# Kernel tuning notes

Hardware: AMD Instinct MI355X
Metric: run time of the kernel (lower is better)

The kernel has to match this reference:

```python
import jax, jax.numpy as jnp
import numpy as np

N, E, D, L = 100000, 640000, 128, 5
BN_EPS = 1e-5


def setup_inputs() -> dict:
    key = jax.random.key(0)
    ks = jax.random.split(key, 10)
    x = jax.random.normal(ks[0], (N, D), jnp.float32)
    edge_index = jax.random.randint(ks[1], (2, E), 0, N, dtype=jnp.int32)
    W1 = jax.random.normal(ks[2], (L, D, 2 * D), jnp.float32) / np.float32(np.sqrt(D))
    b1 = jnp.zeros((L, 2 * D), jnp.float32)
    bn1_g = jnp.ones((L, 2 * D), jnp.float32)
    bn1_b = jnp.zeros((L, 2 * D), jnp.float32)
    bn1_m = 0.1 * jax.random.normal(ks[3], (L, 2 * D), jnp.float32)
    bn1_v = jax.random.uniform(ks[4], (L, 2 * D), jnp.float32) + 0.5
    W2 = jax.random.normal(ks[5], (L, 2 * D, D), jnp.float32) / np.float32(np.sqrt(2 * D))
    b2 = jnp.zeros((L, D), jnp.float32)
    bno_g = jnp.ones((L, D), jnp.float32)
    bno_b = jnp.zeros((L, D), jnp.float32)
    bno_m = 0.1 * jax.random.normal(ks[6], (L, D), jnp.float32)
    bno_v = jax.random.uniform(ks[7], (L, D), jnp.float32) + 0.5
    return {"x": x, "edge_index": edge_index, "W1": W1, "b1": b1,
            "bn1_g": bn1_g, "bn1_b": bn1_b, "bn1_m": bn1_m, "bn1_v": bn1_v,
            "W2": W2, "b2": b2,
            "bno_g": bno_g, "bno_b": bno_b, "bno_m": bno_m, "bno_v": bno_v}


def _bn(z, g, b, m, v):
    # BatchNorm1d in eval mode: running stats
    return (z - m) * jax.lax.rsqrt(v + BN_EPS) * g + b


def reference(x, edge_index, W1, b1, bn1_g, bn1_b, bn1_m, bn1_v,
              W2, b2, bno_g, bno_b, bno_m, bno_v):
    src, dst = edge_index[0], edge_index[1]
    h = x
    for l in range(L):
        # GINConv with eps=0: (1+eps)*h_i + sum_{j->i} h_j
        agg = h + jax.ops.segment_sum(h[src], dst, num_segments=N)  # [N, d]
        z = jax.nn.relu(_bn(agg @ W1[l] + b1[l], bn1_g[l], bn1_b[l], bn1_m[l], bn1_v[l]))
        h = _bn(z @ W2[l] + b2[l], bno_g[l], bno_b[l], bno_m[l], bno_v[l])
        if l != L - 1:
            h = jax.nn.relu(h)
        # dropout is identity in eval mode
    return h
```

## Files before the change

kernel.cpp:

```cpp
#include <hip/hip_runtime.h>

#define ND 100000
#define DD 128
#define HH 256
#define EE 640000
#define LL 5

typedef __attribute__((ext_vector_type(8))) short short8;
typedef __attribute__((ext_vector_type(4))) short short4v;
typedef __attribute__((ext_vector_type(4))) float f32x4;

static __device__ __forceinline__ short f2bf(float f) {
    unsigned u = __builtin_bit_cast(unsigned, f);
    unsigned r = (u + 0x7fffu + ((u >> 16) & 1u)) >> 16;
    return (short)r;
}
static __device__ __forceinline__ float bf2f(short s) {
    unsigned u = ((unsigned)(unsigned short)s) << 16;
    return __builtin_bit_cast(float, u);
}

__global__ __launch_bounds__(256) void setup(
    const float* __restrict__ W1, const float* __restrict__ b1,
    const float* __restrict__ g1, const float* __restrict__ bb1,
    const float* __restrict__ m1, const float* __restrict__ v1,
    const float* __restrict__ W2, const float* __restrict__ b2,
    const float* __restrict__ g2, const float* __restrict__ bb2,
    const float* __restrict__ m2, const float* __restrict__ v2,
    const float* __restrict__ x, const int* __restrict__ dst,
    short* __restrict__ W1p, float* __restrict__ b1e,
    short* __restrict__ W2p, float* __restrict__ b2e,
    short* __restrict__ hb, int* __restrict__ cnt)
{
    int bx = blockIdx.x;
    int tid = threadIdx.x;
    if (bx < 640) {
        int id = bx * 256 + tid;
        if (id < LL * HH * DD) {
            int l = id >> 15;
            int rem = id & 32767;
            {
                int n = rem >> 7, k = rem & 127;
                float s = g1[l * HH + n] * rsqrtf(v1[l * HH + n] + 1e-5f);
                W1p[id] = f2bf(W1[l * 32768 + k * HH + n] * s);
            }
            {
                int n2 = rem >> 8, k2 = rem & 255;
                float s = g2[l * DD + n2] * rsqrtf(v2[l * DD + n2] + 1e-5f);
                W2p[id] = f2bf(W2[l * 32768 + k2 * DD + n2] * s);
            }
        }
        if (id < LL * HH) {
            float s = g1[id] * rsqrtf(v1[id] + 1e-5f);
            b1e[id] = (b1[id] - m1[id]) * s + bb1[id];
        }
        if (id < LL * DD) {
            float s = g2[id] * rsqrtf(v2[id] + 1e-5f);
            b2e[id] = (b2[id] - m2[id]) * s + bb2[id];
        }
    } else if (bx < 13140) {
        int i = (bx - 640) * 256 + tid;
        float4 v = reinterpret_cast<const float4*>(x)[i];
        short4v s;
        s.x = f2bf(v.x); s.y = f2bf(v.y); s.z = f2bf(v.z); s.w = f2bf(v.w);
        reinterpret_cast<short4v*>(hb)[i] = s;
    } else {
        int e = (bx - 13140) * 256 + tid;
        if (e < EE) atomicAdd(&cnt[dst[e]], 1);
    }
}

__global__ __launch_bounds__(256) void scan_block(int* __restrict__ cnt, int* __restrict__ bsum)
{
    __shared__ int buf[256];
    int tid = threadIdx.x;
    int idx = blockIdx.x * 256 + tid;
    int v = (idx < ND) ? cnt[idx] : 0;
    buf[tid] = v;
    __syncthreads();
    int sum = v;
    for (int off = 1; off < 256; off <<= 1) {
        int t = (tid >= off) ? buf[tid - off] : 0;
        __syncthreads();
        sum += t;
        buf[tid] = sum;
        __syncthreads();
    }
    if (idx < ND) cnt[idx] = sum;
    if (tid == 255) bsum[blockIdx.x] = sum;
}

__global__ __launch_bounds__(256) void apply_offs2(const int* __restrict__ cnt,
                                                   const int* __restrict__ bsum,
                                                   int* __restrict__ rowst)
{
    __shared__ int sred[256];
    int tid = threadIdx.x;
    int partial = 0;
    for (int i = tid; i < blockIdx.x; i += 256) partial += bsum[i];
    sred[tid] = partial;
    __syncthreads();
    for (int off = 128; off > 0; off >>= 1) {
        if (tid < off) sred[tid] += sred[tid + off];
        __syncthreads();
    }
    int boff = sred[0];
    int idx = blockIdx.x * 256 + tid;
    if (idx < ND) rowst[idx + 1] = cnt[idx] + boff;
    if (idx == 0) rowst[0] = 0;
}

__global__ __launch_bounds__(256) void fill_csr(const int* __restrict__ src,
                                                const int* __restrict__ dst,
                                                const int* __restrict__ rowstart,
                                                int* __restrict__ cursor,
                                                int* __restrict__ csr)
{
    int e = blockIdx.x * 256 + threadIdx.x;
    if (e < EE) {
        int d = dst[e];
        int p = atomicAdd(&cursor[d], 1);
        csr[rowstart[d] + p] = src[e];
    }
}

__global__ __launch_bounds__(1024, 8) void layer_fused(
    const short* __restrict__ hb_in,
    const int* __restrict__ rowst,
    const int* __restrict__ csr,
    const short* __restrict__ W1l,
    const float* __restrict__ b1l,
    const short* __restrict__ W2l,
    const float* __restrict__ b2l,
    short* __restrict__ hb_out, float* __restrict__ f_out, int last)
{
    __shared__ __attribute__((aligned(16))) short sU[64 * 264];

    const int tid = threadIdx.x;
    const int r0 = blockIdx.x * 64;
    const int wave = tid >> 6;
    const int lane = tid & 63;
    const int quad = lane >> 4;
    const int l16 = lane & 15;

    const int zrow = wave * 16 + l16;
    short8 aw1[4];
    for (int ks = 0; ks < 4; ++ks)
        aw1[ks] = *reinterpret_cast<const short8*>(&W1l[zrow * DD + ks * 32 + quad * 8]);
    float4 bias1 = *reinterpret_cast<const float4*>(&b1l[wave * 16 + quad * 4]);

    {
        int row = tid >> 4;
        int ch = (tid & 15) * 8;
        int grow = r0 + row;
        float acc[8];
        if (grow < ND) {
            short8 h0 = *reinterpret_cast<const short8*>(&hb_in[(size_t)grow * DD + ch]);
            for (int j = 0; j < 8; ++j) acc[j] = bf2f(h0[j]);
            int s = rowst[grow], e = rowst[grow + 1];
            int i = s;
            for (; i + 3 < e; i += 4) {
                int s0 = csr[i], s1 = csr[i + 1], s2 = csr[i + 2], s3 = csr[i + 3];
                short8 a0 = *reinterpret_cast<const short8*>(&hb_in[(size_t)s0 * DD + ch]);
                short8 a1 = *reinterpret_cast<const short8*>(&hb_in[(size_t)s1 * DD + ch]);
                short8 a2 = *reinterpret_cast<const short8*>(&hb_in[(size_t)s2 * DD + ch]);
                short8 a3 = *reinterpret_cast<const short8*>(&hb_in[(size_t)s3 * DD + ch]);
                for (int j = 0; j < 8; ++j)
                    acc[j] += (bf2f(a0[j]) + bf2f(a1[j])) + (bf2f(a2[j]) + bf2f(a3[j]));
            }
            for (; i < e; ++i) {
                short8 a = *reinterpret_cast<const short8*>(&hb_in[(size_t)csr[i] * DD + ch]);
                for (int j = 0; j < 8; ++j) acc[j] += bf2f(a[j]);
            }
        } else {
            for (int j = 0; j < 8; ++j) acc[j] = 0.f;
        }
        short8 o;
        for (int j = 0; j < 8; ++j) o[j] = f2bf(acc[j]);
        *reinterpret_cast<short8*>(&sU[row * 136 + ch]) = o;
    }
    __syncthreads();

    const f32x4 zero4 = {0.f, 0.f, 0.f, 0.f};
    f32x4 acc1[4];
    for (int nt = 0; nt < 4; ++nt) acc1[nt] = zero4;

    for (int ks = 0; ks < 4; ++ks) {
        int kofs = ks * 32 + quad * 8;
        for (int nt = 0; nt < 4; ++nt) {
            short8 bn = *reinterpret_cast<const short8*>(&sU[(nt * 16 + l16) * 136 + kofs]);
            acc1[nt] = __builtin_amdgcn_mfma_f32_16x16x32_bf16(aw1[ks], bn, acc1[nt], 0, 0, 0);
        }
    }
    __syncthreads();

    {
        int zc = wave * 16 + quad * 4;
        for (int nt = 0; nt < 4; ++nt) {
            int node = nt * 16 + l16;
            short4v o;
            o.x = f2bf(fmaxf(acc1[nt][0] + bias1.x, 0.f));
            o.y = f2bf(fmaxf(acc1[nt][1] + bias1.y, 0.f));
            o.z = f2bf(fmaxf(acc1[nt][2] + bias1.z, 0.f));
            o.w = f2bf(fmaxf(acc1[nt][3] + bias1.w, 0.f));
            *reinterpret_cast<short4v*>(&sU[node * 264 + zc]) = o;
        }
    }

    const int ct16 = wave >> 1;
    const int nh = wave & 1;
    const int orow = ct16 * 16 + l16;
    short8 w_cur = *reinterpret_cast<const short8*>(&W2l[orow * HH + quad * 8]);
    float4 bias2 = *reinterpret_cast<const float4*>(&b2l[ct16 * 16 + quad * 4]);
    __syncthreads();

    f32x4 acc2[2];
    for (int nt = 0; nt < 2; ++nt) acc2[nt] = zero4;

    for (int ks = 0; ks < 8; ++ks) {
        short8 w_next;
        if (ks < 7)
            w_next = *reinterpret_cast<const short8*>(&W2l[orow * HH + (ks + 1) * 32 + quad * 8]);
        int kofs = ks * 32 + quad * 8;
        for (int nt = 0; nt < 2; ++nt) {
            int node = nh * 32 + nt * 16 + l16;
            short8 bn = *reinterpret_cast<const short8*>(&sU[node * 264 + kofs]);
            acc2[nt] = __builtin_amdgcn_mfma_f32_16x16x32_bf16(w_cur, bn, acc2[nt], 0, 0, 0);
        }
        w_cur = w_next;
    }

    {
        int oc = ct16 * 16 + quad * 4;
        for (int nt = 0; nt < 2; ++nt) {
            int node = r0 + nh * 32 + nt * 16 + l16;
            if (node < ND) {
                float v0 = acc2[nt][0] + bias2.x;
                float v1 = acc2[nt][1] + bias2.y;
                float v2 = acc2[nt][2] + bias2.z;
                float v3 = acc2[nt][3] + bias2.w;
                if (!last) {
                    short4v o;
                    o.x = f2bf(fmaxf(v0, 0.f));
                    o.y = f2bf(fmaxf(v1, 0.f));
                    o.z = f2bf(fmaxf(v2, 0.f));
                    o.w = f2bf(fmaxf(v3, 0.f));
                    *reinterpret_cast<short4v*>(&hb_out[(size_t)node * DD + oc]) = o;
                } else {
                    float4 st; st.x = v0; st.y = v1; st.z = v2; st.w = v3;
                    *reinterpret_cast<float4*>(&f_out[(size_t)node * DD + oc]) = st;
                }
            }
        }
    }
}

extern "C" void kernel_launch(void* const* d_in, const int* in_sizes, int n_in,
                              void* d_out, int out_size, void* d_ws, size_t ws_size,
                              hipStream_t stream)
{
    const float* x  = (const float*)d_in[0];
    const int* ei   = (const int*)d_in[1];
    const int* src  = ei;
    const int* dst  = ei + EE;
    const float* W1 = (const float*)d_in[2];
    const float* b1 = (const float*)d_in[3];
    const float* g1 = (const float*)d_in[4];
    const float* bb1= (const float*)d_in[5];
    const float* m1 = (const float*)d_in[6];
    const float* v1 = (const float*)d_in[7];
    const float* W2 = (const float*)d_in[8];
    const float* b2 = (const float*)d_in[9];
    const float* g2 = (const float*)d_in[10];
    const float* bb2= (const float*)d_in[11];
    const float* m2 = (const float*)d_in[12];
    const float* v2 = (const float*)d_in[13];

    char* w = (char*)d_ws;
    short* hbufA = (short*)w;
    short* hbufB = (short*)(w + 25600000);
    short* W1p   = (short*)(w + 51200000);
    short* W2p   = (short*)(w + 51527680);
    float* b1e   = (float*)(w + 51855360);
    float* b2e   = (float*)(w + 51860480);
    int*   cnt   = (int*)  (w + 51863040);
    int*   cursor= (int*)  (w + 52263040);
    int*   rowst = (int*)  (w + 52663040);
    int*   csr   = (int*)  (w + 53063072);
    int*   bsum  = (int*)  (w + 55623072);
    float* out   = (float*)d_out;

    hipMemsetAsync(cnt, 0, 800000, stream);
    setup<<<15640, 256, 0, stream>>>(W1, b1, g1, bb1, m1, v1,
                                     W2, b2, g2, bb2, m2, v2,
                                     x, dst, W1p, b1e, W2p, b2e, hbufA, cnt);
    scan_block<<<391, 256, 0, stream>>>(cnt, bsum);
    apply_offs2<<<391, 256, 0, stream>>>(cnt, bsum, rowst);
    fill_csr<<<2500, 256, 0, stream>>>(src, dst, rowst, cursor, csr);

    short* hin = hbufA;
    short* hout = hbufB;
    for (int l = 0; l < LL; ++l) {
        layer_fused<<<1563, 1024, 0, stream>>>(hin, rowst, csr,
                                               W1p + l * 32768, b1e + l * HH,
                                               W2p + l * 32768, b2e + l * DD,
                                               hout, out, (l == LL - 1) ? 1 : 0);
        short* t = hin; hin = hout; hout = t;
    }
}
```

Measured before the change: 551.5 us.

## Shrink fused layer tile to 32 nodes with 512 threads and staged stores

The fused GIN layer kernel now processes 32 nodes per block with 8 waves instead of 64 nodes with 16 waves. Each wave computes a 32x32 tile of the first GEMM, streaming W1 fragments with prefetch rather than holding all of them in registers. Other changes: the gather is software-pipelined one batch of four neighbors ahead, LDS rows are padded with new strides, MFMA loops raise wave priority, and outputs are staged through LDS for coalesced full-row stores. Bounds checks were removed because 100000 divides evenly by 32, and the smaller blocks are meant to improve occupancy and tail balance at the cost of more blocks and more weight loads overall.

```diff
diff --git a/kernel.cpp b/kernel.cpp
--- a/kernel.cpp
+++ b/kernel.cpp
@@ -5,6 +5,11 @@
 #define HH 256
 #define EE 640000
 #define LL 5
+
+#define GS 152
+#define ZS 280
+#define OS 136
+#define OF 132
 
 typedef __attribute__((ext_vector_type(8))) short short8;
 typedef __attribute__((ext_vector_type(4))) short short4v;
@@ -124,7 +129,7 @@
     }
 }
 
-__global__ __launch_bounds__(1024, 8) void layer_fused(
+__global__ __launch_bounds__(512, 8) void layer_fused(
     const short* __restrict__ hb_in,
     const int* __restrict__ rowst,
     const int* __restrict__ csr,
@@ -134,124 +139,186 @@
     const float* __restrict__ b2l,
     short* __restrict__ hb_out, float* __restrict__ f_out, int last)
 {
-    __shared__ __attribute__((aligned(16))) short sU[64 * 264];
+    __shared__ __attribute__((aligned(16))) short sU[32 * ZS];
 
     const int tid = threadIdx.x;
-    const int r0 = blockIdx.x * 64;
-    const int wave = tid >> 6;
+    const int r0 = blockIdx.x * 32;
+    const int w = tid >> 6;
     const int lane = tid & 63;
     const int quad = lane >> 4;
     const int l16 = lane & 15;
 
-    const int zrow = wave * 16 + l16;
-    short8 aw1[4];
-    for (int ks = 0; ks < 4; ++ks)
-        aw1[ks] = *reinterpret_cast<const short8*>(&W1l[zrow * DD + ks * 32 + quad * 8]);
-    float4 bias1 = *reinterpret_cast<const float4*>(&b1l[wave * 16 + quad * 4]);
-
     {
-        int row = tid >> 4;
-        int ch = (tid & 15) * 8;
-        int grow = r0 + row;
+        const int row = tid >> 4;
+        const int ch = (tid & 15) * 8;
+        const int grow = r0 + row;
+        const int s = rowst[grow], e = rowst[grow + 1];
+        short8 h0 = *reinterpret_cast<const short8*>(&hb_in[(size_t)grow * DD + ch]);
         float acc[8];
-        if (grow < ND) {
-            short8 h0 = *reinterpret_cast<const short8*>(&hb_in[(size_t)grow * DD + ch]);
-            for (int j = 0; j < 8; ++j) acc[j] = bf2f(h0[j]);
-            int s = rowst[grow], e = rowst[grow + 1];
-            int i = s;
-            for (; i + 3 < e; i += 4) {
-                int s0 = csr[i], s1 = csr[i + 1], s2 = csr[i + 2], s3 = csr[i + 3];
-                short8 a0 = *reinterpret_cast<const short8*>(&hb_in[(size_t)s0 * DD + ch]);
-                short8 a1 = *reinterpret_cast<const short8*>(&hb_in[(size_t)s1 * DD + ch]);
-                short8 a2 = *reinterpret_cast<const short8*>(&hb_in[(size_t)s2 * DD + ch]);
-                short8 a3 = *reinterpret_cast<const short8*>(&hb_in[(size_t)s3 * DD + ch]);
+        #pragma unroll
+        for (int j = 0; j < 8; ++j) acc[j] = bf2f(h0[j]);
+
+        const int deg = e - s;
+        const int nfull = deg >> 2;
+        const int rem = deg & 3;
+        int i = s;
+        short8 ca[4];
+        if (nfull) {
+            #pragma unroll
+            for (int k = 0; k < 4; ++k)
+                ca[k] = *reinterpret_cast<const short8*>(&hb_in[(size_t)csr[i + k] * DD + ch]);
+            i += 4;
+            for (int b = 1; b < nfull; ++b) {
+                short8 na[4];
+                #pragma unroll
+                for (int k = 0; k < 4; ++k)
+                    na[k] = *reinterpret_cast<const short8*>(&hb_in[(size_t)csr[i + k] * DD + ch]);
+                i += 4;
+                #pragma unroll
                 for (int j = 0; j < 8; ++j)
-                    acc[j] += (bf2f(a0[j]) + bf2f(a1[j])) + (bf2f(a2[j]) + bf2f(a3[j]));
+                    acc[j] += (bf2f(ca[0][j]) + bf2f(ca[1][j])) + (bf2f(ca[2][j]) + bf2f(ca[3][j]));
+                #pragma unroll
+                for (int k = 0; k < 4; ++k) ca[k] = na[k];
             }
-            for (; i < e; ++i) {
-                short8 a = *reinterpret_cast<const short8*>(&hb_in[(size_t)csr[i] * DD + ch]);
-                for (int j = 0; j < 8; ++j) acc[j] += bf2f(a[j]);
-            }
-        } else {
-            for (int j = 0; j < 8; ++j) acc[j] = 0.f;
+        }
+        short8 t0, t1, t2;
+        if (rem > 0) t0 = *reinterpret_cast<const short8*>(&hb_in[(size_t)csr[i] * DD + ch]);
+        if (rem > 1) t1 = *reinterpret_cast<const short8*>(&hb_in[(size_t)csr[i + 1] * DD + ch]);
+        if (rem > 2) t2 = *reinterpret_cast<const short8*>(&hb_in[(size_t)csr[i + 2] * DD + ch]);
+        if (nfull) {
+            #pragma unroll
+            for (int j = 0; j < 8; ++j)
+                acc[j] += (bf2f(ca[0][j]) + bf2f(ca[1][j])) + (bf2f(ca[2][j]) + bf2f(ca[3][j]));
+        }
+        if (rem > 0) {
+            #pragma unroll
+            for (int j = 0; j < 8; ++j) acc[j] += bf2f(t0[j]);
+        }
+        if (rem > 1) {
+            #pragma unroll
+            for (int j = 0; j < 8; ++j) acc[j] += bf2f(t1[j]);
+        }
+        if (rem > 2) {
+            #pragma unroll
+            for (int j = 0; j < 8; ++j) acc[j] += bf2f(t2[j]);
         }
         short8 o;
+        #pragma unroll
         for (int j = 0; j < 8; ++j) o[j] = f2bf(acc[j]);
-        *reinterpret_cast<short8*>(&sU[row * 136 + ch]) = o;
+        *reinterpret_cast<short8*>(&sU[row * GS + ch]) = o;
     }
     __syncthreads();
 
     const f32x4 zero4 = {0.f, 0.f, 0.f, 0.f};
-    f32x4 acc1[4];
-    for (int nt = 0; nt < 4; ++nt) acc1[nt] = zero4;
-
+    f32x4 acc1[2][2];
+    #pragma unroll
+    for (int h = 0; h < 2; ++h)
+        #pragma unroll
+        for (int nt = 0; nt < 2; ++nt) acc1[h][nt] = zero4;
+
+    const int zr0 = w * 32 + l16;
+    short8 a_cur0 = *reinterpret_cast<const short8*>(&W1l[zr0 * DD + quad * 8]);
+    short8 a_cur1 = *reinterpret_cast<const short8*>(&W1l[(zr0 + 16) * DD + quad * 8]);
+
+    __builtin_amdgcn_s_setprio(1);
+    #pragma unroll
     for (int ks = 0; ks < 4; ++ks) {
+        short8 a_n0, a_n1;
+        if (ks < 3) {
+            a_n0 = *reinterpret_cast<const short8*>(&W1l[zr0 * DD + (ks + 1) * 32 + quad * 8]);
+            a_n1 = *reinterpret_cast<const short8*>(&W1l[(zr0 + 16) * DD + (ks + 1) * 32 + quad * 8]);
+        }
         int kofs = ks * 32 + quad * 8;
-        for (int nt = 0; nt < 4; ++nt) {
-            short8 bn = *reinterpret_cast<const short8*>(&sU[(nt * 16 + l16) * 136 + kofs]);
-            acc1[nt] = __builtin_amdgcn_mfma_f32_16x16x32_bf16(aw1[ks], bn, acc1[nt], 0, 0, 0);
-        }
-    }
-    __syncthreads();
-
-    {
-        int zc = wave * 16 + quad * 4;
-        for (int nt = 0; nt < 4; ++nt) {
+        short8 b0 = *reinterpret_cast<const short8*>(&sU[l16 * GS + kofs]);
+        short8 b1 = *reinterpret_cast<const short8*>(&sU[(16 + l16) * GS + kofs]);
+        acc1[0][0] = __builtin_amdgcn_mfma_f32_16x16x32_bf16(a_cur0, b0, acc1[0][0], 0, 0, 0);
+        acc1[0][1] = __builtin_amdgcn_mfma_f32_16x16x32_bf16(a_cur0, b1, acc1[0][1], 0, 0, 0);
+        acc1[1][0] = __builtin_amdgcn_mfma_f32_16x16x32_bf16(a_cur1, b0, acc1[1][0], 0, 0, 0);
+        acc1[1][1] = __builtin_amdgcn_mfma_f32_16x16x32_bf16(a_cur1, b1, acc1[1][1], 0, 0, 0);
+        a_cur0 = a_n0; a_cur1 = a_n1;
+    }
+    __builtin_amdgcn_s_setprio(0);
+
+    float4 bi0 = *reinterpret_cast<const float4*>(&b1l[w * 32 + quad * 4]);
+    float4 bi1 = *reinterpret_cast<const float4*>(&b1l[w * 32 + 16 + quad * 4]);
+    __syncthreads();
+
+    #pragma unroll
+    for (int h = 0; h < 2; ++h) {
+        float4 bi = h ? bi1 : bi0;
+        int zc = w * 32 + h * 16 + quad * 4;
+        #pragma unroll
+        for (int nt = 0; nt < 2; ++nt) {
             int node = nt * 16 + l16;
             short4v o;
-            o.x = f2bf(fmaxf(acc1[nt][0] + bias1.x, 0.f));
-            o.y = f2bf(fmaxf(acc1[nt][1] + bias1.y, 0.f));
-            o.z = f2bf(fmaxf(acc1[nt][2] + bias1.z, 0.f));
-            o.w = f2bf(fmaxf(acc1[nt][3] + bias1.w, 0.f));
-            *reinterpret_cast<short4v*>(&sU[node * 264 + zc]) = o;
-        }
-    }
-
-    const int ct16 = wave >> 1;
-    const int nh = wave & 1;
-    const int orow = ct16 * 16 + l16;
+            o.x = f2bf(fmaxf(acc1[h][nt][0] + bi.x, 0.f));
+            o.y = f2bf(fmaxf(acc1[h][nt][1] + bi.y, 0.f));
+            o.z = f2bf(fmaxf(acc1[h][nt][2] + bi.z, 0.f));
+            o.w = f2bf(fmaxf(acc1[h][nt][3] + bi.w, 0.f));
+            *reinterpret_cast<short4v*>(&sU[node * ZS + zc]) = o;
+        }
+    }
+
+    const int orow = w * 16 + l16;
     short8 w_cur = *reinterpret_cast<const short8*>(&W2l[orow * HH + quad * 8]);
-    float4 bias2 = *reinterpret_cast<const float4*>(&b2l[ct16 * 16 + quad * 4]);
+    float4 bi2 = *reinterpret_cast<const float4*>(&b2l[w * 16 + quad * 4]);
     __syncthreads();
 
     f32x4 acc2[2];
-    for (int nt = 0; nt < 2; ++nt) acc2[nt] = zero4;
-
+    acc2[0] = zero4; acc2[1] = zero4;
+
+    __builtin_amdgcn_s_setprio(1);
+    #pragma unroll
     for (int ks = 0; ks < 8; ++ks) {
         short8 w_next;
         if (ks < 7)
             w_next = *reinterpret_cast<const short8*>(&W2l[orow * HH + (ks + 1) * 32 + quad * 8]);
         int kofs = ks * 32 + quad * 8;
+        short8 b0 = *reinterpret_cast<const short8*>(&sU[l16 * ZS + kofs]);
+        short8 b1 = *reinterpret_cast<const short8*>(&sU[(16 + l16) * ZS + kofs]);
+        acc2[0] = __builtin_amdgcn_mfma_f32_16x16x32_bf16(w_cur, b0, acc2[0], 0, 0, 0);
+        acc2[1] = __builtin_amdgcn_mfma_f32_16x16x32_bf16(w_cur, b1, acc2[1], 0, 0, 0);
+        w_cur = w_next;
+    }
+    __builtin_amdgcn_s_setprio(0);
+    __syncthreads();
+
+    const int oc = w * 16 + quad * 4;
+    if (!last) {
+        #pragma unroll
         for (int nt = 0; nt < 2; ++nt) {
-            int node = nh * 32 + nt * 16 + l16;
-            short8 bn = *reinterpret_cast<const short8*>(&sU[node * 264 + kofs]);
-            acc2[nt] = __builtin_amdgcn_mfma_f32_16x16x32_bf16(w_cur, bn, acc2[nt], 0, 0, 0);
-        }
-        w_cur = w_next;
-    }
-
-    {
-        int oc = ct16 * 16 + quad * 4;
+            int node = nt * 16 + l16;
+            short4v o;
+            o.x = f2bf(fmaxf(acc2[nt][0] + bi2.x, 0.f));
+            o.y = f2bf(fmaxf(acc2[nt][1] + bi2.y, 0.f));
+            o.z = f2bf(fmaxf(acc2[nt][2] + bi2.z, 0.f));
+            o.w = f2bf(fmaxf(acc2[nt][3] + bi2.w, 0.f));
+            *reinterpret_cast<short4v*>(&sU[node * OS + oc]) = o;
+        }
+        __syncthreads();
+        int row = tid >> 4;
+        int c8 = (tid & 15) * 8;
+        short8 v = *reinterpret_cast<const short8*>(&sU[row * OS + c8]);
+        *reinterpret_cast<short8*>(&hb_out[(size_t)(r0 + row) * DD + c8]) = v;
+    } else {
+        float* fU = reinterpret_cast<float*>(sU);
+        #pragma unroll
         for (int nt = 0; nt < 2; ++nt) {
-            int node = r0 + nh * 32 + nt * 16 + l16;
-            if (node < ND) {
-                float v0 = acc2[nt][0] + bias2.x;
-                float v1 = acc2[nt][1] + bias2.y;
-                float v2 = acc2[nt][2] + bias2.z;
-                float v3 = acc2[nt][3] + bias2.w;
-                if (!last) {
-                    short4v o;
-                    o.x = f2bf(fmaxf(v0, 0.f));
-                    o.y = f2bf(fmaxf(v1, 0.f));
-                    o.z = f2bf(fmaxf(v2, 0.f));
-                    o.w = f2bf(fmaxf(v3, 0.f));
-                    *reinterpret_cast<short4v*>(&hb_out[(size_t)node * DD + oc]) = o;
-                } else {
-                    float4 st; st.x = v0; st.y = v1; st.z = v2; st.w = v3;
-                    *reinterpret_cast<float4*>(&f_out[(size_t)node * DD + oc]) = st;
-                }
-            }
-        }
+            int node = nt * 16 + l16;
+            float4 o;
+            o.x = acc2[nt][0] + bi2.x;
+            o.y = acc2[nt][1] + bi2.y;
+            o.z = acc2[nt][2] + bi2.z;
+            o.w = acc2[nt][3] + bi2.w;
+            *reinterpret_cast<float4*>(&fU[node * OF + oc]) = o;
+        }
+        __syncthreads();
+        int row = tid >> 4;
+        int cb = (tid & 15) * 8;
+        float4 v0 = *reinterpret_cast<const float4*>(&fU[row * OF + cb]);
+        float4 v1 = *reinterpret_cast<const float4*>(&fU[row * OF + cb + 4]);
+        *reinterpret_cast<float4*>(&f_out[(size_t)(r0 + row) * DD + cb]) = v0;
+        *reinterpret_cast<float4*>(&f_out[(size_t)(r0 + row) * DD + cb + 4]) = v1;
     }
 }
 
@@ -301,10 +368,10 @@
     short* hin = hbufA;
     short* hout = hbufB;
     for (int l = 0; l < LL; ++l) {
-        layer_fused<<<1563, 1024, 0, stream>>>(hin, rowst, csr,
-                                               W1p + l * 32768, b1e + l * HH,
-                                               W2p + l * 32768, b2e + l * DD,
-                                               hout, out, (l == LL - 1) ? 1 : 0);
+        layer_fused<<<3125, 512, 0, stream>>>(hin, rowst, csr,
+                                              W1p + l * 32768, b1e + l * HH,
+                                              W2p + l * 32768, b2e + l * DD,
+                                              hout, out, (l == LL - 1) ? 1 : 0);
         short* t = hin; hin = hout; hout = t;
     }
 }
```

Result: no change. 549.4 us (-0.4%).

## Switch activations and weights from bf16 to fp16 with packed half math

Applied to the files above, without the earlier changes.

Stores activations and folded weights as fp16 instead of bf16 and uses the f16 MFMA variant. Neighbor aggregation now accumulates directly in packed half8 vectors instead of unpacking to fp32, and conversions use the hardware pack-with-round-toward-zero instruction. LDS row strides are also changed, presumably to reduce bank conflicts. This cuts ALU work in the gather and conversion paths, at the risk of fp16 overflow or precision loss when summing many neighbors in half precision.

```diff
diff --git a/kernel.cpp b/kernel.cpp
--- a/kernel.cpp
+++ b/kernel.cpp
@@ -6,18 +6,22 @@
 #define EE 640000
 #define LL 5
 
+#define GS 152
+#define ZS 280
+
 typedef __attribute__((ext_vector_type(8))) short short8;
 typedef __attribute__((ext_vector_type(4))) short short4v;
 typedef __attribute__((ext_vector_type(4))) float f32x4;
-
-static __device__ __forceinline__ short f2bf(float f) {
-    unsigned u = __builtin_bit_cast(unsigned, f);
-    unsigned r = (u + 0x7fffu + ((u >> 16) & 1u)) >> 16;
-    return (short)r;
-}
-static __device__ __forceinline__ float bf2f(short s) {
-    unsigned u = ((unsigned)(unsigned short)s) << 16;
-    return __builtin_bit_cast(float, u);
+typedef __attribute__((ext_vector_type(8))) _Float16 half8;
+typedef __attribute__((ext_vector_type(4))) _Float16 half4;
+typedef __attribute__((ext_vector_type(2))) _Float16 half2v;
+
+static __device__ __forceinline__ short f2h(float f) {
+    return __builtin_bit_cast(short, (_Float16)f);
+}
+
+static __device__ __forceinline__ half2v pk2(float a, float b) {
+    return __builtin_bit_cast(half2v, __builtin_amdgcn_cvt_pkrtz(a, b));
 }
 
 __global__ __launch_bounds__(256) void setup(
@@ -42,12 +46,12 @@
             {
                 int n = rem >> 7, k = rem & 127;
                 float s = g1[l * HH + n] * rsqrtf(v1[l * HH + n] + 1e-5f);
-                W1p[id] = f2bf(W1[l * 32768 + k * HH + n] * s);
+                W1p[id] = f2h(W1[l * 32768 + k * HH + n] * s);
             }
             {
                 int n2 = rem >> 8, k2 = rem & 255;
                 float s = g2[l * DD + n2] * rsqrtf(v2[l * DD + n2] + 1e-5f);
-                W2p[id] = f2bf(W2[l * 32768 + k2 * DD + n2] * s);
+                W2p[id] = f2h(W2[l * 32768 + k2 * DD + n2] * s);
             }
         }
         if (id < LL * HH) {
@@ -61,9 +65,10 @@
     } else if (bx < 13140) {
         int i = (bx - 640) * 256 + tid;
         float4 v = reinterpret_cast<const float4*>(x)[i];
-        short4v s;
-        s.x = f2bf(v.x); s.y = f2bf(v.y); s.z = f2bf(v.z); s.w = f2bf(v.w);
-        reinterpret_cast<short4v*>(hb)[i] = s;
+        half2v p0 = pk2(v.x, v.y);
+        half2v p1 = pk2(v.z, v.w);
+        half4 hv = __builtin_shufflevector(p0, p1, 0, 1, 2, 3);
+        reinterpret_cast<short4v*>(hb)[i] = __builtin_bit_cast(short4v, hv);
     } else {
         int e = (bx - 13140) * 256 + tid;
         if (e < EE) atomicAdd(&cnt[dst[e]], 1);
@@ -134,7 +139,7 @@
     const float* __restrict__ b2l,
     short* __restrict__ hb_out, float* __restrict__ f_out, int last)
 {
-    __shared__ __attribute__((aligned(16))) short sU[64 * 264];
+    __shared__ __attribute__((aligned(16))) short sU[64 * ZS];
 
     const int tid = threadIdx.x;
     const int r0 = blockIdx.x * 64;
@@ -144,40 +149,43 @@
     const int l16 = lane & 15;
 
     const int zrow = wave * 16 + l16;
-    short8 aw1[4];
+    half8 aw1[4];
     for (int ks = 0; ks < 4; ++ks)
-        aw1[ks] = *reinterpret_cast<const short8*>(&W1l[zrow * DD + ks * 32 + quad * 8]);
+        aw1[ks] = __builtin_bit_cast(half8,
+            *reinterpret_cast<const short8*>(&W1l[zrow * DD + ks * 32 + quad * 8]));
     float4 bias1 = *reinterpret_cast<const float4*>(&b1l[wave * 16 + quad * 4]);
 
     {
         int row = tid >> 4;
         int ch = (tid & 15) * 8;
         int grow = r0 + row;
-        float acc[8];
+        half8 acc = {};
         if (grow < ND) {
-            short8 h0 = *reinterpret_cast<const short8*>(&hb_in[(size_t)grow * DD + ch]);
-            for (int j = 0; j < 8; ++j) acc[j] = bf2f(h0[j]);
+            acc = __builtin_bit_cast(half8,
+                *reinterpret_cast<const short8*>(&hb_in[(size_t)grow * DD + ch]));
             int s = rowst[grow], e = rowst[grow + 1];
             int i = s;
             for (; i + 3 < e; i += 4) {
                 int s0 = csr[i], s1 = csr[i + 1], s2 = csr[i + 2], s3 = csr[i + 3];
-                short8 a0 = *reinterpret_cast<const short8*>(&hb_in[(size_t)s0 * DD + ch]);
-                short8 a1 = *reinterpret_cast<const short8*>(&hb_in[(size_t)s1 * DD + ch]);
-                short8 a2 = *reinterpret_cast<const short8*>(&hb_in[(size_t)s2 * DD + ch]);
-                short8 a3 = *reinterpret_cast<const short8*>(&hb_in[(size_t)s3 * DD + ch]);
-                for (int j = 0; j < 8; ++j)
-                    acc[j] += (bf2f(a0[j]) + bf2f(a1[j])) + (bf2f(a2[j]) + bf2f(a3[j]));
+                half8 a0 = __builtin_bit_cast(half8,
+                    *reinterpret_cast<const short8*>(&hb_in[(size_t)s0 * DD + ch]));
+                half8 a1 = __builtin_bit_cast(half8,
+                    *reinterpret_cast<const short8*>(&hb_in[(size_t)s1 * DD + ch]));
+                half8 a2 = __builtin_bit_cast(half8,
+                    *reinterpret_cast<const short8*>(&hb_in[(size_t)s2 * DD + ch]));
+                half8 a3 = __builtin_bit_cast(half8,
+                    *reinterpret_cast<const short8*>(&hb_in[(size_t)s3 * DD + ch]));
+                half8 s01 = a0 + a1;
+                half8 s23 = a2 + a3;
+                acc = acc + (s01 + s23);
             }
             for (; i < e; ++i) {
-                short8 a = *reinterpret_cast<const short8*>(&hb_in[(size_t)csr[i] * DD + ch]);
-                for (int j = 0; j < 8; ++j) acc[j] += bf2f(a[j]);
-            }
-        } else {
-            for (int j = 0; j < 8; ++j) acc[j] = 0.f;
-        }
-        short8 o;
-        for (int j = 0; j < 8; ++j) o[j] = f2bf(acc[j]);
-        *reinterpret_cast<short8*>(&sU[row * 136 + ch]) = o;
+                half8 a = __builtin_bit_cast(half8,
+                    *reinterpret_cast<const short8*>(&hb_in[(size_t)csr[i] * DD + ch]));
+                acc = acc + a;
+            }
+        }
+        *reinterpret_cast<short8*>(&sU[row * GS + ch]) = __builtin_bit_cast(short8, acc);
     }
     __syncthreads();
 
@@ -188,8 +196,9 @@
     for (int ks = 0; ks < 4; ++ks) {
         int kofs = ks * 32 + quad * 8;
         for (int nt = 0; nt < 4; ++nt) {
-            short8 bn = *reinterpret_cast<const short8*>(&sU[(nt * 16 + l16) * 136 + kofs]);
-            acc1[nt] = __builtin_amdgcn_mfma_f32_16x16x32_bf16(aw1[ks], bn, acc1[nt], 0, 0, 0);
+            half8 bn = __builtin_bit_cast(half8,
+                *reinterpret_cast<const short8*>(&sU[(nt * 16 + l16) * GS + kofs]));
+            acc1[nt] = __builtin_amdgcn_mfma_f32_16x16x32_f16(aw1[ks], bn, acc1[nt], 0, 0, 0);
         }
     }
     __syncthreads();
@@ -198,19 +207,20 @@
         int zc = wave * 16 + quad * 4;
         for (int nt = 0; nt < 4; ++nt) {
             int node = nt * 16 + l16;
-            short4v o;
-            o.x = f2bf(fmaxf(acc1[nt][0] + bias1.x, 0.f));
-            o.y = f2bf(fmaxf(acc1[nt][1] + bias1.y, 0.f));
-            o.z = f2bf(fmaxf(acc1[nt][2] + bias1.z, 0.f));
-            o.w = f2bf(fmaxf(acc1[nt][3] + bias1.w, 0.f));
-            *reinterpret_cast<short4v*>(&sU[node * 264 + zc]) = o;
+            half2v p0 = pk2(fmaxf(acc1[nt][0] + bias1.x, 0.f),
+                            fmaxf(acc1[nt][1] + bias1.y, 0.f));
+            half2v p1 = pk2(fmaxf(acc1[nt][2] + bias1.z, 0.f),
+                            fmaxf(acc1[nt][3] + bias1.w, 0.f));
+            half4 hv = __builtin_shufflevector(p0, p1, 0, 1, 2, 3);
+            *reinterpret_cast<short4v*>(&sU[node * ZS + zc]) = __builtin_bit_cast(short4v, hv);
         }
     }
 
     const int ct16 = wave >> 1;
     const int nh = wave & 1;
     const int orow = ct16 * 16 + l16;
-    short8 w_cur = *reinterpret_cast<const short8*>(&W2l[orow * HH + quad * 8]);
+    half8 w_cur = __builtin_bit_cast(half8,
+        *reinterpret_cast<const short8*>(&W2l[orow * HH + quad * 8]));
     float4 bias2 = *reinterpret_cast<const float4*>(&b2l[ct16 * 16 + quad * 4]);
     __syncthreads();
 
@@ -218,14 +228,16 @@
     for (int nt = 0; nt < 2; ++nt) acc2[nt] = zero4;
 
     for (int ks = 0; ks < 8; ++ks) {
-        short8 w_next;
+        half8 w_next;
         if (ks < 7)
-            w_next = *reinterpret_cast<const short8*>(&W2l[orow * HH + (ks + 1) * 32 + quad * 8]);
+            w_next = __builtin_bit_cast(half8,
+                *reinterpret_cast<const short8*>(&W2l[orow * HH + (ks + 1) * 32 + quad * 8]));
         int kofs = ks * 32 + quad * 8;
         for (int nt = 0; nt < 2; ++nt) {
             int node = nh * 32 + nt * 16 + l16;
-            short8 bn = *reinterpret_cast<const short8*>(&sU[node * 264 + kofs]);
-            acc2[nt] = __builtin_amdgcn_mfma_f32_16x16x32_bf16(w_cur, bn, acc2[nt], 0, 0, 0);
+            half8 bn = __builtin_bit_cast(half8,
+                *reinterpret_cast<const short8*>(&sU[node * ZS + kofs]));
+            acc2[nt] = __builtin_amdgcn_mfma_f32_16x16x32_f16(w_cur, bn, acc2[nt], 0, 0, 0);
         }
         w_cur = w_next;
     }
@@ -240,12 +252,11 @@
                 float v2 = acc2[nt][2] + bias2.z;
                 float v3 = acc2[nt][3] + bias2.w;
                 if (!last) {
-                    short4v o;
-                    o.x = f2bf(fmaxf(v0, 0.f));
-                    o.y = f2bf(fmaxf(v1, 0.f));
-                    o.z = f2bf(fmaxf(v2, 0.f));
-                    o.w = f2bf(fmaxf(v3, 0.f));
-                    *reinterpret_cast<short4v*>(&hb_out[(size_t)node * DD + oc]) = o;
+                    half2v p0 = pk2(fmaxf(v0, 0.f), fmaxf(v1, 0.f));
+                    half2v p1 = pk2(fmaxf(v2, 0.f), fmaxf(v3, 0.f));
+                    half4 hv = __builtin_shufflevector(p0, p1, 0, 1, 2, 3);
+                    *reinterpret_cast<short4v*>(&hb_out[(size_t)node * DD + oc]) =
+                        __builtin_bit_cast(short4v, hv);
                 } else {
                     float4 st; st.x = v0; st.y = v1; st.z = v2; st.w = v3;
                     *reinterpret_cast<float4*>(&f_out[(size_t)node * DD + oc]) = st;
@@ -290,7 +301,7 @@
     int*   bsum  = (int*)  (w + 55623072);
     float* out   = (float*)d_out;
 
-    hipMemsetAsync(cnt, 0, 800000, stream);
+    (void)hipMemsetAsync(cnt, 0, 800000, stream);
     setup<<<15640, 256, 0, stream>>>(W1, b1, g1, bb1, m1, v1,
                                      W2, b2, g2, bb2, m2, v2,
                                      x, dst, W1p, b1e, W2p, b2e, hbufA, cnt);
```

New measurement: 547.6 us. About the same (-0.7%).
